# Optimization experiments

Measured on AMD Instinct MI355X. Metric: run time of the kernel, lower is better.

## Reference

```python
import jax, jax.numpy as jnp
import numpy as np
from jax import lax

P = 16      # n_features
H = 24      # hidden size (hard-coded in module)
B = 8192
T = 168


def setup_inputs() -> dict:
    key = jax.random.key(0)
    ks = jax.random.split(key, 8)
    s_ih = 1.0 / np.sqrt(H)
    return {
        "x": jax.random.normal(ks[0], (B, T, P), dtype=jnp.float32),
        # PyTorch LSTM params: gate order [i, f, g, o], uniform(-1/sqrt(H), 1/sqrt(H))
        "W_ih": jax.random.uniform(ks[1], (4 * H, P), jnp.float32, -s_ih, s_ih),
        "W_hh": jax.random.uniform(ks[2], (4 * H, H), jnp.float32, -s_ih, s_ih),
        "b_ih": jax.random.uniform(ks[3], (4 * H,), jnp.float32, -s_ih, s_ih),
        "b_hh": jax.random.uniform(ks[4], (4 * H,), jnp.float32, -s_ih, s_ih),
        "W_lin": jax.random.uniform(ks[5], (H, H), jnp.float32, -s_ih, s_ih),
        "b_lin": jax.random.uniform(ks[6], (H,), jnp.float32, -s_ih, s_ih),
    }


def _lstm_last_h(x, W_ih, W_hh, b_ih, b_hh):
    # Precompute input-side gate pre-activations for all timesteps: [B, T, 4H]
    xg = jnp.einsum("btp,gp->btg", x, W_ih) + (b_ih + b_hh)
    W_hh_T = W_hh.T  # [H, 4H]
    Bsz = x.shape[0]
    h0 = jnp.zeros((Bsz, H), dtype=x.dtype)
    c0 = jnp.zeros((Bsz, H), dtype=x.dtype)

    def step(carry, xt):
        h, c = carry
        g = xt + h @ W_hh_T  # [B, 4H]
        i = jax.nn.sigmoid(g[:, 0 * H:1 * H])
        f = jax.nn.sigmoid(g[:, 1 * H:2 * H])
        gg = jnp.tanh(g[:, 2 * H:3 * H])
        o = jax.nn.sigmoid(g[:, 3 * H:4 * H])
        c = f * c + i * gg
        h = o * jnp.tanh(c)
        return (h, c), None

    (h_last, _), _ = lax.scan(step, (h0, c0), jnp.swapaxes(xg, 0, 1))
    return h_last  # [B, H]


def reference(x, W_ih, W_hh, b_ih, b_hh, W_lin, b_lin):
    h_last = _lstm_last_h(x, W_ih, W_hh, b_ih, b_hh)
    # tanh over LSTM outputs, then linear head on the last timestep
    out = jnp.tanh(h_last) @ W_lin.T + b_lin  # [B, H]
    return out.reshape(out.shape[0], -1, 1)   # [B, 24, 1]
```

## Files before the change

kernel.cpp:

```cpp
#include <hip/hip_runtime.h>


#define T_STEPS 168
#define P_FEAT  16
#define H_SZ    24
#define TCH     84
#define NB      16

typedef _Float16 half8 __attribute__((ext_vector_type(8)));
typedef _Float16 h2    __attribute__((ext_vector_type(2)));
typedef float    f32x4 __attribute__((ext_vector_type(4)));

__device__ __forceinline__ float rcp_fast(float x) {
#if __has_builtin(__builtin_amdgcn_rcpf)
    return __builtin_amdgcn_rcpf(x);
#else
    return 1.0f / x;
#endif
}
__device__ __forceinline__ float exp2_fast(float x) {
#if __has_builtin(__builtin_amdgcn_exp2f)
    return __builtin_amdgcn_exp2f(x);
#else
    return exp2f(x);
#endif
}
__device__ __forceinline__ float tanh_f(float x) {
    return 1.0f - 2.0f * rcp_fast(1.0f + exp2_fast(x * 2.88539008f));
}
__device__ __forceinline__ h2 pack2(float a, float b) {
    h2 r; r.x = (_Float16)a; r.y = (_Float16)b; return r;
}

__global__ __launch_bounds__(256, 2) void lstm_4w(
    const float* __restrict__ x,
    const float* __restrict__ W_ih,
    const float* __restrict__ W_hh,
    const float* __restrict__ b_ih,
    const float* __restrict__ b_hh,
    const float* __restrict__ W_lin,
    const float* __restrict__ b_lin,
    float* __restrict__ out)
{
    __shared__ __align__(16) _Float16 xs16[NB][TCH][16];
    __shared__ __align__(16) h2       hx[2][4][NB][4];
    __shared__ __align__(16) h2       zblk[8];
    __shared__ __align__(16) float    thbuf[NB][24];

    const int tid  = threadIdx.x;
    const int w    = tid >> 6;
    const int lane = tid & 63;
    const int n    = lane & 15;
    const int q    = lane >> 4;

    float* wstage = reinterpret_cast<float*>(&xs16[0][0][0]);
    for (int idx = tid; idx < 96 * 40; idx += 256) {
        const int j = idx / 40;
        const int k = idx - j * 40;
        wstage[idx] = (k < 24) ? W_hh[j * 24 + k] : W_ih[j * 16 + (k - 24)];
    }
    __syncthreads();

    half8 A1[2], A2[2];
    f32x4 biasf[2];
    #pragma unroll
    for (int s = 0; s < 2; s++) {
        const int mt = 2 * w + s;
        const int p  = n;
        const bool vrow = (p < 12);
        const int grow = vrow ? ((p & 3) * 24 + 8 * (p >> 2) + mt) : 0;
        #pragma unroll
        for (int j = 0; j < 8; j++) {
            const int k = q * 8 + j;
            A1[s][j] = (vrow && k < 24) ? (_Float16)wstage[grow * 40 + k]      : (_Float16)0.0f;
            A2[s][j] = (vrow && k < 16) ? (_Float16)wstage[grow * 40 + 24 + k] : (_Float16)0.0f;
        }
        #pragma unroll
        for (int r = 0; r < 4; r++) {
            const int u = 8 * q + mt;
            biasf[s][r] = (q < 3) ? (b_ih[r * 24 + u] + b_hh[r * 24 + u]) : 0.0f;
        }
    }
    __syncthreads();

    {
        unsigned* hz = reinterpret_cast<unsigned*>(&hx[0][0][0][0]);
        for (int i = tid; i < 512; i += 256) hz[i] = 0u;
        if (tid < 8) reinterpret_cast<unsigned*>(zblk)[tid] = 0u;
    }
    __syncthreads();

    float c[2] = {0.0f, 0.0f};
    float hv[2] = {0.0f, 0.0f};

    const float4* xsrc = reinterpret_cast<const float4*>(x)
                       + (size_t)(blockIdx.x * NB) * (T_STEPS * P_FEAT / 4);

    const _Float16* xrowbase = (q < 2) ? &xs16[n][0][q * 8]
                                       : reinterpret_cast<const _Float16*>(zblk);
    const int xstep = (q < 2) ? 16 : 0;

    int bufp = 0;
    for (int ch = 0; ch < 2; ch++) {
        for (int i = 0; i < 21; i++) {
            const int m   = tid + 256 * i;
            const int b   = m / 336;
            const int rem = m - b * 336;
            const float4 v = xsrc[(size_t)b * 672 + ch * 336 + rem];
            h2* dst = reinterpret_cast<h2*>(&xs16[0][0][0]) + b * 672 + rem * 2;
            dst[0] = pack2(v.x, v.y);
            dst[1] = pack2(v.z, v.w);
        }
        __syncthreads();

        f32x4 gx[2];
        {
            const half8 B2 = *reinterpret_cast<const half8*>(xrowbase);
            #pragma unroll
            for (int s = 0; s < 2; s++)
                gx[s] = __builtin_amdgcn_mfma_f32_16x16x32_f16(A2[s], B2, biasf[s], 0, 0, 0);
        }

        for (int t = 0; t < TCH; t++) {
            const half8 B1 = *reinterpret_cast<const half8*>(&hx[bufp][q][n][0]);
            const int tn = (t + 1 < TCH) ? t + 1 : 0;
            const half8 B2n = *reinterpret_cast<const half8*>(xrowbase + tn * xstep);

            f32x4 g[2];
            #pragma unroll
            for (int s = 0; s < 2; s++)
                g[s] = __builtin_amdgcn_mfma_f32_16x16x32_f16(A1[s], B1, gx[s], 0, 0, 0);
            #pragma unroll
            for (int s = 0; s < 2; s++)
                gx[s] = __builtin_amdgcn_mfma_f32_16x16x32_f16(A2[s], B2n, biasf[s], 0, 0, 0);

            #pragma unroll
            for (int s = 0; s < 2; s++) {
                const float Y  = exp2_fast(g[s][0] * -1.44269504f);
                const float X  = exp2_fast(g[s][1] * -1.44269504f);
                const float Z  = exp2_fast(g[s][2] *  2.88539008f);
                const float V  = exp2_fast(g[s][3] * -1.44269504f);
                const float ax = 1.0f + X;
                const float ay = 1.0f + Y;
                const float az = 1.0f + Z;
                const float num = c[s] * ay * az + ax * (Z - 1.0f);
                const float cn  = num * rcp_fast(ax * ay * az);
                c[s] = cn;
                const float W  = exp2_fast(fminf(cn, 18.0f) * 2.88539008f);
                hv[s] = (W - 1.0f) * rcp_fast((1.0f + V) * (1.0f + W));
            }

            if (q < 3) hx[1 - bufp][q][n][w] = pack2(hv[0], hv[1]);
            bufp ^= 1;
            __syncthreads();
        }
    }

    if (q < 3) {
        thbuf[n][8 * q + 2 * w + 0] = tanh_f(hv[0]);
        thbuf[n][8 * q + 2 * w + 1] = tanh_f(hv[1]);
    }
    __syncthreads();

    if (q < 3) {
        const int batch = blockIdx.x * NB + n;
        #pragma unroll
        for (int s = 0; s < 2; s++) {
            const int u = 8 * q + 2 * w + s;
            const float* wl = &W_lin[u * 24];
            float acc = b_lin[u];
            #pragma unroll
            for (int k = 0; k < 24; k++) acc = fmaf(thbuf[n][k], wl[k], acc);
            out[(size_t)batch * 24 + u] = acc;
        }
    }
}

extern "C" void kernel_launch(void* const* d_in, const int* in_sizes, int n_in,
                              void* d_out, int out_size, void* d_ws, size_t ws_size,
                              hipStream_t stream) {
    const float* x     = (const float*)d_in[0];
    const float* W_ih  = (const float*)d_in[1];
    const float* W_hh  = (const float*)d_in[2];
    const float* b_ih  = (const float*)d_in[3];
    const float* b_hh  = (const float*)d_in[4];
    const float* W_lin = (const float*)d_in[5];
    const float* b_lin = (const float*)d_in[6];
    float* out = (float*)d_out;

    const int B = in_sizes[0] / (T_STEPS * P_FEAT);
    dim3 grid(B / NB), block(256);
    lstm_4w<<<grid, block, 0, stream>>>(x, W_ih, W_hh, b_ih, b_hh, W_lin, b_lin, out);
}
```

Measured before the change: 198.0 us.

## Split LSTM recurrence across two waves with register-forwarded hidden state

Each block now uses two wavefronts instead of four, and each wave computes four gate m-tiles instead of two. Each wave keeps its own half of the hidden-state B operand in registers and reads only the other wave's half from shared memory. This shrinks per-step barrier participation and LDS traffic. The x staging buffer gets a row pad to ease bank conflicts. In exchange there is more serial MFMA and transcendental work per wave, higher register pressure, and launch bounds of one block, which may lower occupancy and latency hiding.

```diff
diff --git a/kernel.cpp b/kernel.cpp
--- a/kernel.cpp
+++ b/kernel.cpp
@@ -3,13 +3,15 @@
 
 #define T_STEPS 168
 #define P_FEAT  16
-#define H_SZ    24
 #define TCH     84
 #define NB      16
+#define BPAD    24
+#define BSTR    (TCH * 16 + BPAD)
 
 typedef _Float16 half8 __attribute__((ext_vector_type(8)));
 typedef _Float16 h2    __attribute__((ext_vector_type(2)));
 typedef float    f32x4 __attribute__((ext_vector_type(4)));
+typedef unsigned uint4v __attribute__((ext_vector_type(4)));
 
 __device__ __forceinline__ float rcp_fast(float x) {
 #if __has_builtin(__builtin_amdgcn_rcpf)
@@ -32,7 +34,7 @@
     h2 r; r.x = (_Float16)a; r.y = (_Float16)b; return r;
 }
 
-__global__ __launch_bounds__(256, 2) void lstm_4w(
+__global__ __launch_bounds__(128, 1) void lstm_2w(
     const float* __restrict__ x,
     const float* __restrict__ W_ih,
     const float* __restrict__ W_hh,
@@ -42,9 +44,9 @@
     const float* __restrict__ b_lin,
     float* __restrict__ out)
 {
-    __shared__ __align__(16) _Float16 xs16[NB][TCH][16];
-    __shared__ __align__(16) h2       hx[2][4][NB][4];
-    __shared__ __align__(16) h2       zblk[8];
+    __shared__ __align__(16) _Float16 xs16[NB * BSTR];
+    __shared__ __align__(16) unsigned hxd[2][4][64];
+    __shared__ __align__(16) _Float16 zblk[16];
     __shared__ __align__(16) float    thbuf[NB][24];
 
     const int tid  = threadIdx.x;
@@ -53,19 +55,19 @@
     const int n    = lane & 15;
     const int q    = lane >> 4;
 
-    float* wstage = reinterpret_cast<float*>(&xs16[0][0][0]);
-    for (int idx = tid; idx < 96 * 40; idx += 256) {
+    float* wstage = reinterpret_cast<float*>(xs16);
+    for (int idx = tid; idx < 96 * 40; idx += 128) {
         const int j = idx / 40;
         const int k = idx - j * 40;
         wstage[idx] = (k < 24) ? W_hh[j * 24 + k] : W_ih[j * 16 + (k - 24)];
     }
     __syncthreads();
 
-    half8 A1[2], A2[2];
-    f32x4 biasf[2];
+    half8 A1[4], A2[4];
+    f32x4 biasf[4];
     #pragma unroll
-    for (int s = 0; s < 2; s++) {
-        const int mt = 2 * w + s;
+    for (int s = 0; s < 4; s++) {
+        const int mt = 4 * w + s;
         const int p  = n;
         const bool vrow = (p < 12);
         const int grow = vrow ? ((p & 3) * 24 + 8 * (p >> 2) + mt) : 0;
@@ -81,61 +83,69 @@
             biasf[s][r] = (q < 3) ? (b_ih[r * 24 + u] + b_hh[r * 24 + u]) : 0.0f;
         }
     }
+    {
+        unsigned* hz = &hxd[0][0][0];
+        for (int i = tid; i < 512; i += 128) hz[i] = 0u;
+        if (tid < 8) reinterpret_cast<unsigned*>(zblk)[tid] = 0u;
+    }
     __syncthreads();
 
-    {
-        unsigned* hz = reinterpret_cast<unsigned*>(&hx[0][0][0][0]);
-        for (int i = tid; i < 512; i += 256) hz[i] = 0u;
-        if (tid < 8) reinterpret_cast<unsigned*>(zblk)[tid] = 0u;
-    }
-    __syncthreads();
-
-    float c[2] = {0.0f, 0.0f};
-    float hv[2] = {0.0f, 0.0f};
+    float c[4]  = {0.0f, 0.0f, 0.0f, 0.0f};
+    float hv[4] = {0.0f, 0.0f, 0.0f, 0.0f};
+    unsigned od0 = 0u, od1 = 0u;
 
     const float4* xsrc = reinterpret_cast<const float4*>(x)
                        + (size_t)(blockIdx.x * NB) * (T_STEPS * P_FEAT / 4);
 
-    const _Float16* xrowbase = (q < 2) ? &xs16[n][0][q * 8]
-                                       : reinterpret_cast<const _Float16*>(zblk);
+    const _Float16* xrowbase = (q < 2) ? &xs16[n * BSTR + q * 8] : zblk;
     const int xstep = (q < 2) ? 16 : 0;
+
+    const int pjj = w ? 0 : 2;
 
     int bufp = 0;
     for (int ch = 0; ch < 2; ch++) {
-        for (int i = 0; i < 21; i++) {
-            const int m   = tid + 256 * i;
+        for (int i = 0; i < 42; i++) {
+            const int m   = tid + 128 * i;
             const int b   = m / 336;
             const int rem = m - b * 336;
             const float4 v = xsrc[(size_t)b * 672 + ch * 336 + rem];
-            h2* dst = reinterpret_cast<h2*>(&xs16[0][0][0]) + b * 672 + rem * 2;
+            h2* dst = reinterpret_cast<h2*>(xs16) + b * (BSTR / 2) + rem * 2;
             dst[0] = pack2(v.x, v.y);
             dst[1] = pack2(v.z, v.w);
         }
         __syncthreads();
 
-        f32x4 gx[2];
+        f32x4 gx[4];
         {
             const half8 B2 = *reinterpret_cast<const half8*>(xrowbase);
             #pragma unroll
-            for (int s = 0; s < 2; s++)
+            for (int s = 0; s < 4; s++)
                 gx[s] = __builtin_amdgcn_mfma_f32_16x16x32_f16(A2[s], B2, biasf[s], 0, 0, 0);
         }
 
         for (int t = 0; t < TCH; t++) {
-            const half8 B1 = *reinterpret_cast<const half8*>(&hx[bufp][q][n][0]);
+            const unsigned pd0 = hxd[bufp][pjj + 0][lane];
+            const unsigned pd1 = hxd[bufp][pjj + 1][lane];
+            uint4v bw;
+            bw.x = w ? pd0 : od0;
+            bw.y = w ? pd1 : od1;
+            bw.z = w ? od0 : pd0;
+            bw.w = w ? od1 : pd1;
+            const half8 B1 = __builtin_bit_cast(half8, bw);
+
             const int tn = (t + 1 < TCH) ? t + 1 : 0;
             const half8 B2n = *reinterpret_cast<const half8*>(xrowbase + tn * xstep);
 
-            f32x4 g[2];
-            #pragma unroll
-            for (int s = 0; s < 2; s++)
+            f32x4 g[4];
+            #pragma unroll
+            for (int s = 0; s < 4; s++)
                 g[s] = __builtin_amdgcn_mfma_f32_16x16x32_f16(A1[s], B1, gx[s], 0, 0, 0);
             #pragma unroll
-            for (int s = 0; s < 2; s++)
+            for (int s = 0; s < 4; s++)
                 gx[s] = __builtin_amdgcn_mfma_f32_16x16x32_f16(A2[s], B2n, biasf[s], 0, 0, 0);
 
             #pragma unroll
-            for (int s = 0; s < 2; s++) {
+            for (int s = 0; s < 4; s++) {
                 const float Y  = exp2_fast(g[s][0] * -1.44269504f);
                 const float X  = exp2_fast(g[s][1] * -1.44269504f);
                 const float Z  = exp2_fast(g[s][2] *  2.88539008f);
@@ -150,23 +160,29 @@
                 hv[s] = (W - 1.0f) * rcp_fast((1.0f + V) * (1.0f + W));
             }
 
-            if (q < 3) hx[1 - bufp][q][n][w] = pack2(hv[0], hv[1]);
+            od0 = __builtin_bit_cast(unsigned, pack2(hv[0], hv[1]));
+            od1 = __builtin_bit_cast(unsigned, pack2(hv[2], hv[3]));
+            if (q < 3) {
+                hxd[1 - bufp][2 * w + 0][lane] = od0;
+                hxd[1 - bufp][2 * w + 1][lane] = od1;
+            }
             bufp ^= 1;
             __syncthreads();
         }
     }
 
     if (q < 3) {
-        thbuf[n][8 * q + 2 * w + 0] = tanh_f(hv[0]);
-        thbuf[n][8 * q + 2 * w + 1] = tanh_f(hv[1]);
+        #pragma unroll
+        for (int s = 0; s < 4; s++)
+            thbuf[n][8 * q + 4 * w + s] = tanh_f(hv[s]);
     }
     __syncthreads();
 
     if (q < 3) {
         const int batch = blockIdx.x * NB + n;
         #pragma unroll
-        for (int s = 0; s < 2; s++) {
-            const int u = 8 * q + 2 * w + s;
+        for (int s = 0; s < 4; s++) {
+            const int u = 8 * q + 4 * w + s;
             const float* wl = &W_lin[u * 24];
             float acc = b_lin[u];
             #pragma unroll
@@ -189,6 +205,6 @@
     float* out = (float*)d_out;
 
     const int B = in_sizes[0] / (T_STEPS * P_FEAT);
-    dim3 grid(B / NB), block(256);
-    lstm_4w<<<grid, block, 0, stream>>>(x, W_ih, W_hh, b_ih, b_hh, W_lin, b_lin, out);
-}
+    dim3 grid(B / NB), block(128);
+    lstm_2w<<<grid, block, 0, stream>>>(x, W_ih, W_hh, b_ih, b_hh, W_lin, b_lin, out);
+}
```

Measured after the change: 265.8 us. +34.2%, slower.

## Split LSTM recurrence across eight waves with one gate tile each

Applied to the files above, without the earlier changes.

Doubles the block to 512 threads so each of eight waves owns a single 16-row gate tile instead of two, halving the per-wave MFMA and transcendental work on the serial timestep critical path. The hidden-state exchange buffer becomes per-wave half scalars. The x staging buffer gets a padded per-batch stride, apparently to reduce LDS bank conflicts. The cost is a wider per-step __syncthreads across eight waves, and launch bounds that target four blocks per CU, which may constrain registers.

```diff
diff --git a/kernel.cpp b/kernel.cpp
--- a/kernel.cpp
+++ b/kernel.cpp
@@ -3,9 +3,10 @@
 
 #define T_STEPS 168
 #define P_FEAT  16
-#define H_SZ    24
 #define TCH     84
 #define NB      16
+#define BPAD    24
+#define BSTR    (TCH * 16 + BPAD)
 
 typedef _Float16 half8 __attribute__((ext_vector_type(8)));
 typedef _Float16 h2    __attribute__((ext_vector_type(2)));
@@ -32,7 +33,7 @@
     h2 r; r.x = (_Float16)a; r.y = (_Float16)b; return r;
 }
 
-__global__ __launch_bounds__(256, 2) void lstm_4w(
+__global__ __launch_bounds__(512, 4) void lstm_8w(
     const float* __restrict__ x,
     const float* __restrict__ W_ih,
     const float* __restrict__ W_hh,
@@ -42,9 +43,9 @@
     const float* __restrict__ b_lin,
     float* __restrict__ out)
 {
-    __shared__ __align__(16) _Float16 xs16[NB][TCH][16];
-    __shared__ __align__(16) h2       hx[2][4][NB][4];
-    __shared__ __align__(16) h2       zblk[8];
+    __shared__ __align__(16) _Float16 xs16[NB * BSTR];
+    __shared__ __align__(16) _Float16 hx[2][4][NB][8];
+    __shared__ __align__(16) _Float16 zblk[16];
     __shared__ __align__(16) float    thbuf[NB][24];
 
     const int tid  = threadIdx.x;
@@ -53,72 +54,68 @@
     const int n    = lane & 15;
     const int q    = lane >> 4;
 
-    float* wstage = reinterpret_cast<float*>(&xs16[0][0][0]);
-    for (int idx = tid; idx < 96 * 40; idx += 256) {
+    float* wstage = reinterpret_cast<float*>(xs16);
+    for (int idx = tid; idx < 96 * 40; idx += 512) {
         const int j = idx / 40;
         const int k = idx - j * 40;
         wstage[idx] = (k < 24) ? W_hh[j * 24 + k] : W_ih[j * 16 + (k - 24)];
     }
     __syncthreads();
 
-    half8 A1[2], A2[2];
-    f32x4 biasf[2];
-    #pragma unroll
-    for (int s = 0; s < 2; s++) {
-        const int mt = 2 * w + s;
+    half8 A1, A2;
+    f32x4 biasf;
+    {
+        const int mt = w;
         const int p  = n;
         const bool vrow = (p < 12);
         const int grow = vrow ? ((p & 3) * 24 + 8 * (p >> 2) + mt) : 0;
         #pragma unroll
         for (int j = 0; j < 8; j++) {
             const int k = q * 8 + j;
-            A1[s][j] = (vrow && k < 24) ? (_Float16)wstage[grow * 40 + k]      : (_Float16)0.0f;
-            A2[s][j] = (vrow && k < 16) ? (_Float16)wstage[grow * 40 + 24 + k] : (_Float16)0.0f;
+            A1[j] = (vrow && k < 24) ? (_Float16)wstage[grow * 40 + k]      : (_Float16)0.0f;
+            A2[j] = (vrow && k < 16) ? (_Float16)wstage[grow * 40 + 24 + k] : (_Float16)0.0f;
         }
         #pragma unroll
         for (int r = 0; r < 4; r++) {
             const int u = 8 * q + mt;
-            biasf[s][r] = (q < 3) ? (b_ih[r * 24 + u] + b_hh[r * 24 + u]) : 0.0f;
+            biasf[r] = (q < 3) ? (b_ih[r * 24 + u] + b_hh[r * 24 + u]) : 0.0f;
         }
     }
-    __syncthreads();
-
     {
         unsigned* hz = reinterpret_cast<unsigned*>(&hx[0][0][0][0]);
-        for (int i = tid; i < 512; i += 256) hz[i] = 0u;
+        for (int i = tid; i < 512; i += 512) hz[i] = 0u;
         if (tid < 8) reinterpret_cast<unsigned*>(zblk)[tid] = 0u;
     }
     __syncthreads();
 
-    float c[2] = {0.0f, 0.0f};
-    float hv[2] = {0.0f, 0.0f};
+    float c  = 0.0f;
+    float hv = 0.0f;
 
     const float4* xsrc = reinterpret_cast<const float4*>(x)
                        + (size_t)(blockIdx.x * NB) * (T_STEPS * P_FEAT / 4);
 
-    const _Float16* xrowbase = (q < 2) ? &xs16[n][0][q * 8]
-                                       : reinterpret_cast<const _Float16*>(zblk);
+    const _Float16* xrowbase = (q < 2) ? &xs16[n * BSTR + q * 8] : zblk;
     const int xstep = (q < 2) ? 16 : 0;
 
     int bufp = 0;
     for (int ch = 0; ch < 2; ch++) {
-        for (int i = 0; i < 21; i++) {
-            const int m   = tid + 256 * i;
-            const int b   = m / 336;
-            const int rem = m - b * 336;
-            const float4 v = xsrc[(size_t)b * 672 + ch * 336 + rem];
-            h2* dst = reinterpret_cast<h2*>(&xs16[0][0][0]) + b * 672 + rem * 2;
-            dst[0] = pack2(v.x, v.y);
-            dst[1] = pack2(v.z, v.w);
+        for (int i = 0; i < 11; i++) {
+            const int m = tid + 512 * i;
+            if (m < 5376) {
+                const int b   = m / 336;
+                const int rem = m - b * 336;
+                const float4 v = xsrc[(size_t)b * 672 + ch * 336 + rem];
+                h2* dst = reinterpret_cast<h2*>(xs16) + b * (BSTR / 2) + rem * 2;
+                dst[0] = pack2(v.x, v.y);
+                dst[1] = pack2(v.z, v.w);
+            }
         }
         __syncthreads();
 
-        f32x4 gx[2];
+        f32x4 gx;
         {
             const half8 B2 = *reinterpret_cast<const half8*>(xrowbase);
-            #pragma unroll
-            for (int s = 0; s < 2; s++)
-                gx[s] = __builtin_amdgcn_mfma_f32_16x16x32_f16(A2[s], B2, biasf[s], 0, 0, 0);
+            gx = __builtin_amdgcn_mfma_f32_16x16x32_f16(A2, B2, biasf, 0, 0, 0);
         }
 
         for (int t = 0; t < TCH; t++) {
@@ -126,53 +123,41 @@
             const int tn = (t + 1 < TCH) ? t + 1 : 0;
             const half8 B2n = *reinterpret_cast<const half8*>(xrowbase + tn * xstep);
 
-            f32x4 g[2];
-            #pragma unroll
-            for (int s = 0; s < 2; s++)
-                g[s] = __builtin_amdgcn_mfma_f32_16x16x32_f16(A1[s], B1, gx[s], 0, 0, 0);
-            #pragma unroll
-            for (int s = 0; s < 2; s++)
-                gx[s] = __builtin_amdgcn_mfma_f32_16x16x32_f16(A2[s], B2n, biasf[s], 0, 0, 0);
+            f32x4 g = __builtin_amdgcn_mfma_f32_16x16x32_f16(A1, B1, gx, 0, 0, 0);
+            gx = __builtin_amdgcn_mfma_f32_16x16x32_f16(A2, B2n, biasf, 0, 0, 0);
 
-            #pragma unroll
-            for (int s = 0; s < 2; s++) {
-                const float Y  = exp2_fast(g[s][0] * -1.44269504f);
-                const float X  = exp2_fast(g[s][1] * -1.44269504f);
-                const float Z  = exp2_fast(g[s][2] *  2.88539008f);
-                const float V  = exp2_fast(g[s][3] * -1.44269504f);
+            {
+                const float Y  = exp2_fast(g[0] * -1.44269504f);
+                const float X  = exp2_fast(g[1] * -1.44269504f);
+                const float Z  = exp2_fast(g[2] *  2.88539008f);
+                const float V  = exp2_fast(g[3] * -1.44269504f);
                 const float ax = 1.0f + X;
                 const float ay = 1.0f + Y;
                 const float az = 1.0f + Z;
-                const float num = c[s] * ay * az + ax * (Z - 1.0f);
+                const float num = c * ay * az + ax * (Z - 1.0f);
                 const float cn  = num * rcp_fast(ax * ay * az);
-                c[s] = cn;
+                c = cn;
                 const float W  = exp2_fast(fminf(cn, 18.0f) * 2.88539008f);
-                hv[s] = (W - 1.0f) * rcp_fast((1.0f + V) * (1.0f + W));
+                hv = (W - 1.0f) * rcp_fast((1.0f + V) * (1.0f + W));
             }
 
-            if (q < 3) hx[1 - bufp][q][n][w] = pack2(hv[0], hv[1]);
+            if (q < 3) hx[1 - bufp][q][n][w] = (_Float16)hv;
             bufp ^= 1;
             __syncthreads();
         }
     }
 
-    if (q < 3) {
-        thbuf[n][8 * q + 2 * w + 0] = tanh_f(hv[0]);
-        thbuf[n][8 * q + 2 * w + 1] = tanh_f(hv[1]);
-    }
+    if (q < 3) thbuf[n][8 * q + w] = tanh_f(hv);
     __syncthreads();
 
     if (q < 3) {
         const int batch = blockIdx.x * NB + n;
+        const int u = 8 * q + w;
+        const float* wl = &W_lin[u * 24];
+        float acc = b_lin[u];
         #pragma unroll
-        for (int s = 0; s < 2; s++) {
-            const int u = 8 * q + 2 * w + s;
-            const float* wl = &W_lin[u * 24];
-            float acc = b_lin[u];
-            #pragma unroll
-            for (int k = 0; k < 24; k++) acc = fmaf(thbuf[n][k], wl[k], acc);
-            out[(size_t)batch * 24 + u] = acc;
-        }
+        for (int k = 0; k < 24; k++) acc = fmaf(thbuf[n][k], wl[k], acc);
+        out[(size_t)batch * 24 + u] = acc;
     }
 }
 
@@ -189,6 +174,6 @@
     float* out = (float*)d_out;
 
     const int B = in_sizes[0] / (T_STEPS * P_FEAT);
-    dim3 grid(B / NB), block(256);
-    lstm_4w<<<grid, block, 0, stream>>>(x, W_ih, W_hh, b_ih, b_hh, W_lin, b_lin, out);
+    dim3 grid(B / NB), block(512);
+    lstm_8w<<<grid, block, 0, stream>>>(x, W_ih, W_hh, b_ih, b_hh, W_lin, b_lin, out);
 }
```

Result: no change. 195.9 us (-1.0%).

## Run each 16-sequence group in one wavefront with register-resident hidden state

Applied to the files above, without the earlier changes.

Each wavefront now owns 16 batch rows and all 24 hidden units, computing 6 MFMA tiles per step. The hidden state is packed straight into the MFMA B operand within lanes, so the per-timestep shared-memory exchange and block barrier go away. x is read directly from global memory with a three-deep register prefetch instead of being staged through LDS. In exchange, each wave carries more registers, runs more MFMAs per step on a serial critical path, and launch bounds drop to 128 threads with one block.

```diff
diff --git a/kernel.cpp b/kernel.cpp
--- a/kernel.cpp
+++ b/kernel.cpp
@@ -3,12 +3,8 @@
 
 #define T_STEPS 168
 #define P_FEAT  16
-#define H_SZ    24
-#define TCH     84
-#define NB      16
 
 typedef _Float16 half8 __attribute__((ext_vector_type(8)));
-typedef _Float16 h2    __attribute__((ext_vector_type(2)));
 typedef float    f32x4 __attribute__((ext_vector_type(4)));
 
 __device__ __forceinline__ float rcp_fast(float x) {
@@ -28,11 +24,8 @@
 __device__ __forceinline__ float tanh_f(float x) {
     return 1.0f - 2.0f * rcp_fast(1.0f + exp2_fast(x * 2.88539008f));
 }
-__device__ __forceinline__ h2 pack2(float a, float b) {
-    h2 r; r.x = (_Float16)a; r.y = (_Float16)b; return r;
-}
 
-__global__ __launch_bounds__(256, 2) void lstm_4w(
+__global__ __launch_bounds__(128, 1) void lstm_bf(
     const float* __restrict__ x,
     const float* __restrict__ W_ih,
     const float* __restrict__ W_hh,
@@ -42,137 +35,123 @@
     const float* __restrict__ b_lin,
     float* __restrict__ out)
 {
-    __shared__ __align__(16) _Float16 xs16[NB][TCH][16];
-    __shared__ __align__(16) h2       hx[2][4][NB][4];
-    __shared__ __align__(16) h2       zblk[8];
-    __shared__ __align__(16) float    thbuf[NB][24];
+    __shared__ float thbuf[2][16][25];
 
     const int tid  = threadIdx.x;
-    const int w    = tid >> 6;
+    const int wv   = tid >> 6;
     const int lane = tid & 63;
     const int n    = lane & 15;
     const int q    = lane >> 4;
+    const int batch = blockIdx.x * 32 + wv * 16 + n;
 
-    float* wstage = reinterpret_cast<float*>(&xs16[0][0][0]);
-    for (int idx = tid; idx < 96 * 40; idx += 256) {
-        const int j = idx / 40;
-        const int k = idx - j * 40;
-        wstage[idx] = (k < 24) ? W_hh[j * 24 + k] : W_ih[j * 16 + (k - 24)];
+    half8 A1[6], A2[6];
+    f32x4 biasf[6];
+    #pragma unroll
+    for (int tau = 0; tau < 6; tau++) {
+        const int grow = (n & 3) * 24 + 6 * (n >> 2) + tau;
+        #pragma unroll
+        for (int j = 0; j < 8; j++) {
+            A1[tau][j] = (j < 6) ? (_Float16)W_hh[grow * 24 + 6 * q + j] : (_Float16)0.0f;
+            const int k = 8 * q + j;
+            A2[tau][j] = (k < 16) ? (_Float16)W_ih[grow * 16 + k] : (_Float16)0.0f;
+        }
+        const int u = 6 * q + tau;
+        #pragma unroll
+        for (int r = 0; r < 4; r++)
+            biasf[tau][r] = b_ih[r * 24 + u] + b_hh[r * 24 + u];
     }
+
+    float c[6]  = {0.0f, 0.0f, 0.0f, 0.0f, 0.0f, 0.0f};
+    float hv[6] = {0.0f, 0.0f, 0.0f, 0.0f, 0.0f, 0.0f};
+    half8 B1 = {};
+
+    const float* xrow = x + (size_t)batch * (T_STEPS * P_FEAT) + 8 * q;
+
+    float4 xa0 = {0,0,0,0}, xa1 = {0,0,0,0};
+    float4 xb0 = {0,0,0,0}, xb1 = {0,0,0,0};
+    float4 xc0 = {0,0,0,0}, xc1 = {0,0,0,0};
+
+    auto xload = [&](int t, float4& r0, float4& r1) {
+        if (q < 2) {
+            const float4* p = reinterpret_cast<const float4*>(xrow + (size_t)t * P_FEAT);
+            r0 = p[0];
+            r1 = p[1];
+        }
+    };
+    auto mkB2 = [&](const float4& r0, const float4& r1) -> half8 {
+        half8 b = {};
+        if (q < 2) {
+            b[0] = (_Float16)r0.x; b[1] = (_Float16)r0.y;
+            b[2] = (_Float16)r0.z; b[3] = (_Float16)r0.w;
+            b[4] = (_Float16)r1.x; b[5] = (_Float16)r1.y;
+            b[6] = (_Float16)r1.z; b[7] = (_Float16)r1.w;
+        }
+        return b;
+    };
+
+    f32x4 gx[6];
+
+    auto do_step = [&](const half8 B2n) {
+        f32x4 g[6];
+        #pragma unroll
+        for (int s = 0; s < 6; s++)
+            g[s] = __builtin_amdgcn_mfma_f32_16x16x32_f16(A1[s], B1, gx[s], 0, 0, 0);
+        #pragma unroll
+        for (int s = 0; s < 6; s++)
+            gx[s] = __builtin_amdgcn_mfma_f32_16x16x32_f16(A2[s], B2n, biasf[s], 0, 0, 0);
+        #pragma unroll
+        for (int s = 0; s < 6; s++) {
+            const float Y  = exp2_fast(g[s][0] * -1.44269504f);
+            const float X  = exp2_fast(g[s][1] * -1.44269504f);
+            const float Z  = exp2_fast(g[s][2] *  2.88539008f);
+            const float V  = exp2_fast(g[s][3] * -1.44269504f);
+            const float ax = 1.0f + X;
+            const float ay = 1.0f + Y;
+            const float az = 1.0f + Z;
+            const float num = c[s] * ay * az + ax * (Z - 1.0f);
+            const float cn  = num * rcp_fast(ax * ay * az);
+            c[s] = cn;
+            const float W  = exp2_fast(fminf(cn, 18.0f) * 2.88539008f);
+            hv[s] = (W - 1.0f) * rcp_fast((1.0f + V) * (1.0f + W));
+        }
+        B1[0] = (_Float16)hv[0]; B1[1] = (_Float16)hv[1];
+        B1[2] = (_Float16)hv[2]; B1[3] = (_Float16)hv[3];
+        B1[4] = (_Float16)hv[4]; B1[5] = (_Float16)hv[5];
+    };
+
+    xload(0, xa0, xa1);
+    xload(1, xb0, xb1);
+    xload(2, xc0, xc1);
+    {
+        const half8 B20 = mkB2(xa0, xa1);
+        #pragma unroll
+        for (int s = 0; s < 6; s++)
+            gx[s] = __builtin_amdgcn_mfma_f32_16x16x32_f16(A2[s], B20, biasf[s], 0, 0, 0);
+    }
+    xload(3, xa0, xa1);
+
+    for (int t = 0; t < T_STEPS; t += 3) {
+        do_step(mkB2(xb0, xb1));
+        { const int tn = (t + 4 < T_STEPS) ? t + 4 : 0; xload(tn, xb0, xb1); }
+        do_step(mkB2(xc0, xc1));
+        { const int tn = (t + 5 < T_STEPS) ? t + 5 : 0; xload(tn, xc0, xc1); }
+        do_step(mkB2(xa0, xa1));
+        { const int tn = (t + 6 < T_STEPS) ? t + 6 : 0; xload(tn, xa0, xa1); }
+    }
+
+    #pragma unroll
+    for (int tau = 0; tau < 6; tau++)
+        thbuf[wv][n][6 * q + tau] = tanh_f(hv[tau]);
     __syncthreads();
 
-    half8 A1[2], A2[2];
-    f32x4 biasf[2];
     #pragma unroll
-    for (int s = 0; s < 2; s++) {
-        const int mt = 2 * w + s;
-        const int p  = n;
-        const bool vrow = (p < 12);
-        const int grow = vrow ? ((p & 3) * 24 + 8 * (p >> 2) + mt) : 0;
+    for (int tau = 0; tau < 6; tau++) {
+        const int u = 6 * q + tau;
+        float acc = b_lin[u];
         #pragma unroll
-        for (int j = 0; j < 8; j++) {
-            const int k = q * 8 + j;
-            A1[s][j] = (vrow && k < 24) ? (_Float16)wstage[grow * 40 + k]      : (_Float16)0.0f;
-            A2[s][j] = (vrow && k < 16) ? (_Float16)wstage[grow * 40 + 24 + k] : (_Float16)0.0f;
-        }
-        #pragma unroll
-        for (int r = 0; r < 4; r++) {
-            const int u = 8 * q + mt;
-            biasf[s][r] = (q < 3) ? (b_ih[r * 24 + u] + b_hh[r * 24 + u]) : 0.0f;
-        }
-    }
-    __syncthreads();
-
-    {
-        unsigned* hz = reinterpret_cast<unsigned*>(&hx[0][0][0][0]);
-        for (int i = tid; i < 512; i += 256) hz[i] = 0u;
-        if (tid < 8) reinterpret_cast<unsigned*>(zblk)[tid] = 0u;
-    }
-    __syncthreads();
-
-    float c[2] = {0.0f, 0.0f};
-    float hv[2] = {0.0f, 0.0f};
-
-    const float4* xsrc = reinterpret_cast<const float4*>(x)
-                       + (size_t)(blockIdx.x * NB) * (T_STEPS * P_FEAT / 4);
-
-    const _Float16* xrowbase = (q < 2) ? &xs16[n][0][q * 8]
-                                       : reinterpret_cast<const _Float16*>(zblk);
-    const int xstep = (q < 2) ? 16 : 0;
-
-    int bufp = 0;
-    for (int ch = 0; ch < 2; ch++) {
-        for (int i = 0; i < 21; i++) {
-            const int m   = tid + 256 * i;
-            const int b   = m / 336;
-            const int rem = m - b * 336;
-            const float4 v = xsrc[(size_t)b * 672 + ch * 336 + rem];
-            h2* dst = reinterpret_cast<h2*>(&xs16[0][0][0]) + b * 672 + rem * 2;
-            dst[0] = pack2(v.x, v.y);
-            dst[1] = pack2(v.z, v.w);
-        }
-        __syncthreads();
-
-        f32x4 gx[2];
-        {
-            const half8 B2 = *reinterpret_cast<const half8*>(xrowbase);
-            #pragma unroll
-            for (int s = 0; s < 2; s++)
-                gx[s] = __builtin_amdgcn_mfma_f32_16x16x32_f16(A2[s], B2, biasf[s], 0, 0, 0);
-        }
-
-        for (int t = 0; t < TCH; t++) {
-            const half8 B1 = *reinterpret_cast<const half8*>(&hx[bufp][q][n][0]);
-            const int tn = (t + 1 < TCH) ? t + 1 : 0;
-            const half8 B2n = *reinterpret_cast<const half8*>(xrowbase + tn * xstep);
-
-            f32x4 g[2];
-            #pragma unroll
-            for (int s = 0; s < 2; s++)
-                g[s] = __builtin_amdgcn_mfma_f32_16x16x32_f16(A1[s], B1, gx[s], 0, 0, 0);
-            #pragma unroll
-            for (int s = 0; s < 2; s++)
-                gx[s] = __builtin_amdgcn_mfma_f32_16x16x32_f16(A2[s], B2n, biasf[s], 0, 0, 0);
-
-            #pragma unroll
-            for (int s = 0; s < 2; s++) {
-                const float Y  = exp2_fast(g[s][0] * -1.44269504f);
-                const float X  = exp2_fast(g[s][1] * -1.44269504f);
-                const float Z  = exp2_fast(g[s][2] *  2.88539008f);
-                const float V  = exp2_fast(g[s][3] * -1.44269504f);
-                const float ax = 1.0f + X;
-                const float ay = 1.0f + Y;
-                const float az = 1.0f + Z;
-                const float num = c[s] * ay * az + ax * (Z - 1.0f);
-                const float cn  = num * rcp_fast(ax * ay * az);
-                c[s] = cn;
-                const float W  = exp2_fast(fminf(cn, 18.0f) * 2.88539008f);
-                hv[s] = (W - 1.0f) * rcp_fast((1.0f + V) * (1.0f + W));
-            }
-
-            if (q < 3) hx[1 - bufp][q][n][w] = pack2(hv[0], hv[1]);
-            bufp ^= 1;
-            __syncthreads();
-        }
-    }
-
-    if (q < 3) {
-        thbuf[n][8 * q + 2 * w + 0] = tanh_f(hv[0]);
-        thbuf[n][8 * q + 2 * w + 1] = tanh_f(hv[1]);
-    }
-    __syncthreads();
-
-    if (q < 3) {
-        const int batch = blockIdx.x * NB + n;
-        #pragma unroll
-        for (int s = 0; s < 2; s++) {
-            const int u = 8 * q + 2 * w + s;
-            const float* wl = &W_lin[u * 24];
-            float acc = b_lin[u];
-            #pragma unroll
-            for (int k = 0; k < 24; k++) acc = fmaf(thbuf[n][k], wl[k], acc);
-            out[(size_t)batch * 24 + u] = acc;
-        }
+        for (int k = 0; k < 24; k++)
+            acc = fmaf(thbuf[wv][n][k], W_lin[u * 24 + k], acc);
+        out[(size_t)batch * 24 + u] = acc;
     }
 }
 
@@ -189,6 +168,6 @@
     float* out = (float*)d_out;
 
     const int B = in_sizes[0] / (T_STEPS * P_FEAT);
-    dim3 grid(B / NB), block(256);
-    lstm_4w<<<grid, block, 0, stream>>>(x, W_ih, W_hh, b_ih, b_hh, W_lin, b_lin, out);
+    dim3 grid(B / 32), block(128);
+    lstm_bf<<<grid, block, 0, stream>>>(x, W_ih, W_hh, b_ih, b_hh, W_lin, b_lin, out);
 }
```

Measured after the change: 247.6 us. 1.25x slower.
